# Optimization experiments

Measured on AMD Instinct MI355X. Metric: run time of the kernel, lower is better.

## Reference

```python
import jax, jax.numpy as jnp
import numpy as np

NEG_SLOPE = 0.2

def gat_conv(x, edge_index, W, a_src, a_dst, b, heads, out_ch, concat):
    # PyG GATConv (add_self_loops=True, eval mode / no dropout)
    N = x.shape[0]
    loop = jnp.arange(N, dtype=edge_index.dtype)
    src = jnp.concatenate([edge_index[0], loop])
    dst = jnp.concatenate([edge_index[1], loop])
    h = (x @ W.T).reshape(N, heads, out_ch)            # [N,H,C]
    alpha_s = (h * a_src).sum(-1)                      # [N,H]
    alpha_d = (h * a_dst).sum(-1)                      # [N,H]
    e = jax.nn.leaky_relu(alpha_s[src] + alpha_d[dst], NEG_SLOPE)  # [E,H]
    # segment softmax over incoming edges of each dst node
    m = jax.ops.segment_max(e, dst, num_segments=N)
    e = jnp.exp(e - m[dst])
    denom = jax.ops.segment_sum(e, dst, num_segments=N)
    alpha = e / (denom[dst] + 1e-16)                   # [E,H]
    msg = h[src] * alpha[..., None]                    # [E,H,C]
    out = jax.ops.segment_sum(msg, dst, num_segments=N)  # [N,H,C]
    out = out.reshape(N, heads * out_ch) if concat else out.mean(axis=1)
    return out + b


def setup_inputs() -> dict:
    key = jax.random.key(0)
    ks = jax.random.split(key, 16)
    N, E, F_in, HID, H, OUT = 20000, 320000, 512, 256, 8, 128
    C = HID // H  # 32 channels per head
    x = jax.random.normal(ks[0], (N, F_in), dtype=jnp.float32)
    edge_index = jax.random.randint(ks[1], (2, E), 0, N, dtype=jnp.int32)
    s = 0.05
    inp = {
        'x': x, 'edge_index': edge_index,
        # layer 0: F_in -> H*C, concat
        'W0': jax.random.normal(ks[2], (H * C, F_in)) * s,
        'a_src0': jax.random.normal(ks[3], (1, H, C)) * s,
        'a_dst0': jax.random.normal(ks[4], (1, H, C)) * s,
        'b0': jnp.zeros((H * C,), jnp.float32),
        # layer 1: H*C -> H*C, concat
        'W1': jax.random.normal(ks[5], (H * C, H * C)) * s,
        'a_src1': jax.random.normal(ks[6], (1, H, C)) * s,
        'a_dst1': jax.random.normal(ks[7], (1, H, C)) * s,
        'b1': jnp.zeros((H * C,), jnp.float32),
        # layer 2: H*C -> OUT, 1 head, concat=False
        'W2': jax.random.normal(ks[8], (OUT, H * C)) * s,
        'a_src2': jax.random.normal(ks[9], (1, 1, OUT)) * s,
        'a_dst2': jax.random.normal(ks[10], (1, 1, OUT)) * s,
        'b2': jnp.zeros((OUT,), jnp.float32),
    }
    return inp


def reference(x, edge_index, W0, a_src0, a_dst0, b0, W1, a_src1, a_dst1, b1,
              W2, a_src2, a_dst2, b2):
    H, C, OUT = 8, 32, 128
    h = gat_conv(x, edge_index, W0, a_src0, a_dst0, b0, H, C, True)
    h = jax.nn.relu(h)
    h = gat_conv(h, edge_index, W1, a_src1, a_dst1, b1, H, C, True)
    h = jax.nn.relu(h)
    h_pen = h  # h_list[-1]
    h = gat_conv(h, edge_index, W2, a_src2, a_dst2, b2, 1, OUT, False)
    return (h_pen, h)
```

## Files before the change

### kernel.cpp

```cpp
#include <hip/hip_runtime.h>
#include <hip/hip_bf16.h>


using bf16 = __hip_bfloat16;

typedef __attribute__((ext_vector_type(8))) short bf16x8;
typedef __attribute__((ext_vector_type(4))) short short4v;
typedef __attribute__((ext_vector_type(4))) float f32x4;
typedef __attribute__((ext_vector_type(2))) float f32x2;
typedef __attribute__((ext_vector_type(2))) unsigned int uint2v;

__device__ __forceinline__ float u2f(unsigned u) { union { float f; unsigned u; } c; c.u = u; return c.f; }
__device__ __forceinline__ unsigned f2u(float x) { union { float f; unsigned u; } c; c.f = x; return c.u; }
__device__ __forceinline__ short bfbits(float x) {
  unsigned xu = f2u(x);
  return (short)((xu + 0x7FFF + ((xu >> 16) & 1)) >> 16);
}

__global__ void hist_kernel(const int* __restrict__ ei, int E, int N, int* __restrict__ cnt) {
  int e = blockIdx.x * 256 + threadIdx.x;
  if (e >= E + N) return;
  int dst = (e < E) ? ei[E + e] : (e - E);
  atomicAdd(&cnt[dst], 1);
}

__global__ __launch_bounds__(1024) void scan_kernel(const int* __restrict__ cnt,
                                                    int* __restrict__ row_start, int N) {
  __shared__ int part[1024];
  int t = threadIdx.x;
  int chunk = (N + 1023) / 1024;
  int lo = t * chunk; if (lo > N) lo = N;
  int hi = lo + chunk; if (hi > N) hi = N;
  int s = 0;
  for (int i = lo; i < hi; ++i) s += cnt[i];
  part[t] = s;
  __syncthreads();
  for (int off = 1; off < 1024; off <<= 1) {
    int add = (t >= off) ? part[t - off] : 0;
    __syncthreads();
    part[t] += add;
    __syncthreads();
  }
  int run = part[t] - s;
  for (int i = lo; i < hi; ++i) { row_start[i] = run; run += cnt[i]; }
  if (t == 1023) row_start[N] = part[1023];
}

__global__ void scatter_kernel(const int* __restrict__ ei, int E, int N,
                               const int* __restrict__ row_start, int* __restrict__ cursor,
                               int* __restrict__ csr_src) {
  int e = blockIdx.x * 256 + threadIdx.x;
  if (e >= E + N) return;
  int src, dst;
  if (e < E) { src = ei[e]; dst = ei[E + e]; }
  else       { src = e - E; dst = e - E; }
  int pos = atomicAdd(&cursor[dst], 1);
  csr_src[row_start[dst] + pos] = src;
}

__global__ void split3_kernel(const float* __restrict__ W0, const float* __restrict__ W1,
                              const float* __restrict__ W2,
                              unsigned short* __restrict__ W0h, unsigned short* __restrict__ W0l,
                              unsigned short* __restrict__ W1h, unsigned short* __restrict__ W1l,
                              unsigned short* __restrict__ W2h, unsigned short* __restrict__ W2l,
                              int n0_4, int n1_4, int n2_4) {
  int i = blockIdx.x * 256 + threadIdx.x;
  const float* in; unsigned short *hi, *lo; int idx;
  if (i < n0_4)                { in = W0; hi = W0h; lo = W0l; idx = i; }
  else if (i < n0_4 + n1_4)    { in = W1; hi = W1h; lo = W1l; idx = i - n0_4; }
  else if (i < n0_4 + n1_4 + n2_4) { in = W2; hi = W2h; lo = W2l; idx = i - n0_4 - n1_4; }
  else return;
  f32x4 v = *(const f32x4*)(in + (size_t)idx * 4);
  short4v h, l;
#pragma unroll
  for (int k = 0; k < 4; ++k) {
    short hb = bfbits(v[k]);
    h[k] = hb;
    l[k] = bfbits(v[k] - u2f(((unsigned)(unsigned short)hb) << 16));
  }
  *(short4v*)(hi + (size_t)idx * 4) = h;
  *(short4v*)(lo + (size_t)idx * 4) = l;
}

#define LDP 40

__device__ __forceinline__ bf16x8 make_frag(const short* S, int row, int g) {
  short4v klo = *(const short4v*)&S[row * LDP + g * 4];
  short4v khi = *(const short4v*)&S[row * LDP + 16 + g * 4];
  bf16x8 r;
#pragma unroll
  for (int i = 0; i < 4; ++i) { r[i] = klo[i]; r[i + 4] = khi[i]; }
  return r;
}

template <bool FUSE8, bool WF32>
__global__ __launch_bounds__(256) void gemm_mfma(const float* __restrict__ Af,
                                                 const unsigned short* __restrict__ Bhg,
                                                 const unsigned short* __restrict__ Blg,
                                                 const float* __restrict__ Asrc,
                                                 const float* __restrict__ Adst,
                                                 float* __restrict__ as_,
                                                 float* __restrict__ ad_,
                                                 float* __restrict__ C,
                                                 unsigned short* __restrict__ C16,
                                                 int M, int Nn, int K, int NB) {
  int id = blockIdx.x;
  int r8 = id & 7;
  int q  = id >> 3;
  int bn = q % NB;
  int bm = r8 + 8 * (q / NB);
  if (bm * 64 >= M) return;

  __shared__ short Ah[64 * LDP];
  __shared__ short Al[64 * LDP];
  __shared__ short Bh[64 * LDP];
  __shared__ short Bl[64 * LDP];
  int t = threadIdx.x;
  int w = t >> 6, l = t & 63;
  int g = l >> 4, lr = l & 15;

  f32x4 acc[4];
#pragma unroll
  for (int j = 0; j < 4; ++j) acc[j] = (f32x4)(0.f);

  int srow = t >> 2;
  int sseg = (t & 3) * 8;
  int gm = bm * 64 + srow;
  int gn = bn * 64 + srow;
  const float* Abase = Af + (size_t)gm * K + sseg;
  const unsigned short* Bhb = Bhg + (size_t)gn * K + sseg;
  const unsigned short* Blb = Blg + (size_t)gn * K + sseg;

  f32x4 va0 = (f32x4)(0.f), va1 = (f32x4)(0.f);
  int4 vbh, vbl;
  vbh = *(const int4*)(Bhb);
  vbl = *(const int4*)(Blb);
  if (gm < M) { va0 = *(const f32x4*)(Abase); va1 = *(const f32x4*)(Abase + 4); }

  for (int kt = 0; kt < K; kt += 32) {
    short4v h0, l0, h1, l1;
#pragma unroll
    for (int i = 0; i < 4; ++i) {
      short hb0 = bfbits(va0[i]);
      l0[i] = bfbits(va0[i] - u2f(((unsigned)(unsigned short)hb0) << 16));
      h0[i] = hb0;
      short hb1 = bfbits(va1[i]);
      l1[i] = bfbits(va1[i] - u2f(((unsigned)(unsigned short)hb1) << 16));
      h1[i] = hb1;
    }
    __syncthreads();
    *(int4*)&Bh[srow * LDP + sseg] = vbh;
    *(int4*)&Bl[srow * LDP + sseg] = vbl;
    *(short4v*)&Ah[srow * LDP + sseg]     = h0;
    *(short4v*)&Ah[srow * LDP + sseg + 4] = h1;
    *(short4v*)&Al[srow * LDP + sseg]     = l0;
    *(short4v*)&Al[srow * LDP + sseg + 4] = l1;
    __syncthreads();

    if (kt + 32 < K) {
      int k2 = kt + 32;
      vbh = *(const int4*)(Bhb + k2);
      vbl = *(const int4*)(Blb + k2);
      if (gm < M) { va0 = *(const f32x4*)(Abase + k2); va1 = *(const f32x4*)(Abase + k2 + 4); }
    }

    int arow = w * 16 + lr;
    bf16x8 ah = make_frag(Ah, arow, g);
    bf16x8 al = make_frag(Al, arow, g);
#pragma unroll
    for (int j = 0; j < 4; ++j) {
      int brow = j * 16 + lr;
      bf16x8 bh = make_frag(Bh, brow, g);
      bf16x8 bl = make_frag(Bl, brow, g);
      acc[j] = __builtin_amdgcn_mfma_f32_16x16x32_bf16(ah, bh, acc[j], 0, 0, 0);
      acc[j] = __builtin_amdgcn_mfma_f32_16x16x32_bf16(al, bh, acc[j], 0, 0, 0);
      acc[j] = __builtin_amdgcn_mfma_f32_16x16x32_bf16(ah, bl, acc[j], 0, 0, 0);
    }
  }

#pragma unroll
  for (int j = 0; j < 4; ++j) {
#pragma unroll
    for (int r = 0; r < 4; ++r) {
      int row = bm * 64 + w * 16 + g * 4 + r;
      int col = bn * 64 + j * 16 + lr;
      if (row < M) {
        float v = acc[j][r];
        if constexpr (WF32) C[(size_t)row * Nn + col] = v;
        C16[(size_t)row * Nn + col] = (unsigned short)bfbits(v);
      }
    }
  }

  if constexpr (FUSE8) {
    float cs[4], cd[4];
#pragma unroll
    for (int j = 0; j < 4; ++j) {
      cs[j] = Asrc[bn * 64 + j * 16 + lr];
      cd[j] = Adst[bn * 64 + j * 16 + lr];
    }
#pragma unroll
    for (int r = 0; r < 4; ++r) {
      float sA0 = acc[0][r] * cs[0] + acc[1][r] * cs[1];
      float sA1 = acc[2][r] * cs[2] + acc[3][r] * cs[3];
      float sD0 = acc[0][r] * cd[0] + acc[1][r] * cd[1];
      float sD1 = acc[2][r] * cd[2] + acc[3][r] * cd[3];
#pragma unroll
      for (int mask = 1; mask < 16; mask <<= 1) {
        sA0 += __shfl_xor(sA0, mask);
        sA1 += __shfl_xor(sA1, mask);
        sD0 += __shfl_xor(sD0, mask);
        sD1 += __shfl_xor(sD1, mask);
      }
      if (lr == 0) {
        int row = bm * 64 + w * 16 + g * 4 + r;
        if (row < M) {
          as_[row * 8 + bn * 2]     = sA0;
          as_[row * 8 + bn * 2 + 1] = sA1;
          ad_[row * 8 + bn * 2]     = sD0;
          ad_[row * 8 + bn * 2 + 1] = sD1;
        }
      }
    }
  }
}

template <int H, int C>
__global__ __launch_bounds__(64) void alpha_kernel(const float* __restrict__ Hb,
                                                   const float* __restrict__ a_src,
                                                   const float* __restrict__ a_dst,
                                                   float* __restrict__ as_,
                                                   float* __restrict__ ad_, int N) {
  constexpr int HC = H * C;
  constexpr int EPL = HC / 64;
  constexpr int LPH = 64 / H;
  int n = blockIdx.x;
  int l = threadIdx.x;
  const float* row = Hb + (size_t)n * HC + l * EPL;
  float s1 = 0.f, s2 = 0.f;
  if constexpr (EPL == 4) {
    f32x4 v = *(const f32x4*)row;
    f32x4 a1 = *(const f32x4*)(a_src + l * 4);
    f32x4 a2 = *(const f32x4*)(a_dst + l * 4);
#pragma unroll
    for (int k = 0; k < 4; ++k) { s1 += v[k] * a1[k]; s2 += v[k] * a2[k]; }
  } else {
    f32x2 v = *(const f32x2*)row;
    f32x2 a1 = *(const f32x2*)(a_src + l * 2);
    f32x2 a2 = *(const f32x2*)(a_dst + l * 2);
#pragma unroll
    for (int k = 0; k < 2; ++k) { s1 += v[k] * a1[k]; s2 += v[k] * a2[k]; }
  }
#pragma unroll
  for (int mask = 1; mask < LPH; mask <<= 1) {
    s1 += __shfl_xor(s1, mask);
    s2 += __shfl_xor(s2, mask);
  }
  if ((l & (LPH - 1)) == 0) {
    int h = l / LPH;
    as_[n * H + h] = s1;
    ad_[n * H + h] = s2;
  }
}

template <int H, int C, bool RELU>
__global__ __launch_bounds__(64) void agg_kernel(const unsigned short* __restrict__ Hb16,
                                                 const float* __restrict__ as_,
                                                 const float* __restrict__ ad_,
                                                 const int* __restrict__ row_start,
                                                 const int* __restrict__ csr_src,
                                                 const float* __restrict__ bias,
                                                 float* __restrict__ out, int N) {
  int n = blockIdx.x;
  if (n >= N) return;
  int l = threadIdx.x;
  int s = row_start[n], e = row_start[n + 1];

  constexpr int LPH = 64 / H;
  constexpr int CPL = C / LPH;
  constexpr int HC = H * C;
  int h2 = l / LPH;
  int cb = (l % LPH) * CPL;
  float ad2 = ad_[n * H + h2];

  float acc[CPL];
#pragma unroll
  for (int c = 0; c < CPL; ++c) acc[c] = 0.f;
  float denom = 0.f;

  int j = s;
  for (; j + 1 < e; j += 2) {
    int s0 = csr_src[j], s1v = csr_src[j + 1];
    float x0 = as_[s0 * H + h2] + ad2;
    float x1 = as_[s1v * H + h2] + ad2;
    x0 = x0 > 0.f ? x0 : 0.2f * x0;
    x1 = x1 > 0.f ? x1 : 0.2f * x1;
    float p0 = __expf(x0), p1 = __expf(x1);
    denom += p0 + p1;
    const unsigned short* hp0 = Hb16 + (size_t)s0 * HC + h2 * C + cb;
    const unsigned short* hp1 = Hb16 + (size_t)s1v * HC + h2 * C + cb;
    if constexpr (CPL == 4) {
      uint2v u0 = *(const uint2v*)hp0;
      uint2v u1 = *(const uint2v*)hp1;
#pragma unroll
      for (int c = 0; c < 2; ++c) {
        acc[2 * c]     += p0 * u2f(u0[c] << 16)         + p1 * u2f(u1[c] << 16);
        acc[2 * c + 1] += p0 * u2f(u0[c] & 0xFFFF0000u) + p1 * u2f(u1[c] & 0xFFFF0000u);
      }
    } else {
      unsigned u0 = *(const unsigned*)hp0;
      unsigned u1 = *(const unsigned*)hp1;
      acc[0] += p0 * u2f(u0 << 16)         + p1 * u2f(u1 << 16);
      acc[1] += p0 * u2f(u0 & 0xFFFF0000u) + p1 * u2f(u1 & 0xFFFF0000u);
    }
  }
  if (j < e) {
    int s0 = csr_src[j];
    float x0 = as_[s0 * H + h2] + ad2;
    x0 = x0 > 0.f ? x0 : 0.2f * x0;
    float p0 = __expf(x0);
    denom += p0;
    const unsigned short* hp0 = Hb16 + (size_t)s0 * HC + h2 * C + cb;
    if constexpr (CPL == 4) {
      uint2v u0 = *(const uint2v*)hp0;
#pragma unroll
      for (int c = 0; c < 2; ++c) {
        acc[2 * c]     += p0 * u2f(u0[c] << 16);
        acc[2 * c + 1] += p0 * u2f(u0[c] & 0xFFFF0000u);
      }
    } else {
      unsigned u0 = *(const unsigned*)hp0;
      acc[0] += p0 * u2f(u0 << 16);
      acc[1] += p0 * u2f(u0 & 0xFFFF0000u);
    }
  }

  float inv = 1.f / (denom + 1e-16f);
#pragma unroll
  for (int c = 0; c < CPL; ++c) {
    float v = acc[c] * inv + bias[h2 * C + cb + c];
    if (RELU) v = fmaxf(v, 0.f);
    out[(size_t)n * HC + h2 * C + cb + c] = v;
  }
}

extern "C" void kernel_launch(void* const* d_in, const int* in_sizes, int n_in,
                              void* d_out, int out_size, void* d_ws, size_t ws_size,
                              hipStream_t stream) {
  const float* x    = (const float*)d_in[0];
  const int*   ei   = (const int*)d_in[1];
  const float* W0   = (const float*)d_in[2];
  const float* asr0 = (const float*)d_in[3];
  const float* adt0 = (const float*)d_in[4];
  const float* b0   = (const float*)d_in[5];
  const float* W1   = (const float*)d_in[6];
  const float* asr1 = (const float*)d_in[7];
  const float* adt1 = (const float*)d_in[8];
  const float* b1   = (const float*)d_in[9];
  const float* W2   = (const float*)d_in[10];
  const float* asr2 = (const float*)d_in[11];
  const float* adt2 = (const float*)d_in[12];
  const float* b2   = (const float*)d_in[13];

  const int FIN = 512, HID = 256, OUTC = 128;
  int N = in_sizes[0] / FIN;
  int E = in_sizes[1] / 2;
  int Etot = E + N;

  char* ws = (char*)d_ws;
  size_t off = 0;
  auto alloc = [&](size_t bytes) -> void* {
    void* p = ws + off;
    off = (off + bytes + 255) & ~(size_t)255;
    return p;
  };
  int* cnt       = (int*)alloc((size_t)N * 4);
  int* cursor    = (int*)alloc((size_t)N * 4);
  int* row_start = (int*)alloc((size_t)(N + 1) * 4);
  int* csr_src   = (int*)alloc((size_t)Etot * 4);
  float* as_     = (float*)alloc((size_t)N * 8 * 4);
  float* ad_     = (float*)alloc((size_t)N * 8 * 4);
  float* Hb      = (float*)alloc((size_t)N * HID * 4);
  unsigned short* Hb16 = (unsigned short*)alloc((size_t)N * HID * 2);
  float* act     = (float*)alloc((size_t)N * HID * 4);
  unsigned short* W0h = (unsigned short*)alloc((size_t)HID * FIN * 2);
  unsigned short* W0l = (unsigned short*)alloc((size_t)HID * FIN * 2);
  unsigned short* W1h = (unsigned short*)alloc((size_t)HID * HID * 2);
  unsigned short* W1l = (unsigned short*)alloc((size_t)HID * HID * 2);
  unsigned short* W2h = (unsigned short*)alloc((size_t)OUTC * HID * 2);
  unsigned short* W2l = (unsigned short*)alloc((size_t)OUTC * HID * 2);

  float* hpen = (float*)d_out;
  float* out2 = (float*)d_out + (size_t)N * HID;

  int n0_4 = HID * FIN / 4, n1_4 = HID * HID / 4, n2_4 = OUTC * HID / 4;
  int nsplit = n0_4 + n1_4 + n2_4;
  split3_kernel<<<(nsplit + 255) / 256, 256, 0, stream>>>(W0, W1, W2, W0h, W0l, W1h, W1l,
                                                          W2h, W2l, n0_4, n1_4, n2_4);

  (void)hipMemsetAsync(cnt, 0, (size_t)((char*)cursor - (char*)cnt) + (size_t)N * 4, stream);
  int eb = (Etot + 255) / 256;
  hist_kernel<<<eb, 256, 0, stream>>>(ei, E, N, cnt);
  scan_kernel<<<1, 1024, 0, stream>>>(cnt, row_start, N);
  scatter_kernel<<<eb, 256, 0, stream>>>(ei, E, N, row_start, cursor, csr_src);

  int mb = (N + 63) / 64;
  int mb8 = (mb + 7) / 8;
  int grid4 = 8 * 4 * mb8;
  int grid2 = 8 * 2 * mb8;

  gemm_mfma<true, false><<<grid4, 256, 0, stream>>>(x, W0h, W0l, asr0, adt0, as_, ad_,
                                                    nullptr, Hb16, N, HID, FIN, 4);
  agg_kernel<8, 32, true><<<N, 64, 0, stream>>>(Hb16, as_, ad_, row_start, csr_src, b0,
                                                act, N);

  gemm_mfma<true, false><<<grid4, 256, 0, stream>>>(act, W1h, W1l, asr1, adt1, as_, ad_,
                                                    nullptr, Hb16, N, HID, HID, 4);
  agg_kernel<8, 32, true><<<N, 64, 0, stream>>>(Hb16, as_, ad_, row_start, csr_src, b1,
                                                hpen, N);

  gemm_mfma<false, true><<<grid2, 256, 0, stream>>>(hpen, W2h, W2l, nullptr, nullptr,
                                                    nullptr, nullptr, Hb, Hb16,
                                                    N, OUTC, HID, 2);
  alpha_kernel<1, 128><<<N, 64, 0, stream>>>(Hb, asr2, adt2, as_, ad_, N);
  agg_kernel<1, 128, false><<<N, 64, 0, stream>>>(Hb16, as_, ad_, row_start, csr_src, b2,
                                                  out2, N);
}
```

Measured before the change: 230.6 us.

## Fuse layer-2 attention logits into GEMM epilogue via atomics; unroll aggregation by four

The last-layer GEMM now computes per-row source and destination attention dot products in its epilogue and accumulates them with atomicAdd across the two column blocks. This removes the fp32 output write, the separate alpha kernel and its reread of that buffer. Small zeroing kernels are added before the GEMM to clear the accumulators. The aggregation loop is also unrolled from 2 to 4 edges per step to expose more memory-level parallelism, at the cost of more registers. Accumulating with atomics makes the summation order nondeterministic.

```diff
diff --git a/kernel.cpp b/kernel.cpp
--- a/kernel.cpp
+++ b/kernel.cpp
@@ -82,6 +82,11 @@
   *(short4v*)(lo + (size_t)idx * 4) = l;
 }
 
+__global__ void zero_f32_kernel(float* __restrict__ p, int n) {
+  int i = blockIdx.x * 256 + threadIdx.x;
+  if (i < n) p[i] = 0.f;
+}
+
 #define LDP 40
 
 __device__ __forceinline__ bf16x8 make_frag(const short* S, int row, int g) {
@@ -93,7 +98,7 @@
   return r;
 }
 
-template <bool FUSE8, bool WF32>
+template <bool FUSE8, bool FUSE1>
 __global__ __launch_bounds__(256) void gemm_mfma(const float* __restrict__ Af,
                                                  const unsigned short* __restrict__ Bhg,
                                                  const unsigned short* __restrict__ Blg,
@@ -101,7 +106,6 @@
                                                  const float* __restrict__ Adst,
                                                  float* __restrict__ as_,
                                                  float* __restrict__ ad_,
-                                                 float* __restrict__ C,
                                                  unsigned short* __restrict__ C16,
                                                  int M, int Nn, int K, int NB) {
   int id = blockIdx.x;
@@ -132,9 +136,8 @@
   const unsigned short* Blb = Blg + (size_t)gn * K + sseg;
 
   f32x4 va0 = (f32x4)(0.f), va1 = (f32x4)(0.f);
-  int4 vbh, vbl;
-  vbh = *(const int4*)(Bhb);
-  vbl = *(const int4*)(Blb);
+  int4 vbh = *(const int4*)(Bhb);
+  int4 vbl = *(const int4*)(Blb);
   if (gm < M) { va0 = *(const f32x4*)(Abase); va1 = *(const f32x4*)(Abase + 4); }
 
   for (int kt = 0; kt < K; kt += 32) {
@@ -184,11 +187,7 @@
     for (int r = 0; r < 4; ++r) {
       int row = bm * 64 + w * 16 + g * 4 + r;
       int col = bn * 64 + j * 16 + lr;
-      if (row < M) {
-        float v = acc[j][r];
-        if constexpr (WF32) C[(size_t)row * Nn + col] = v;
-        C16[(size_t)row * Nn + col] = (unsigned short)bfbits(v);
-      }
+      if (row < M) C16[(size_t)row * Nn + col] = (unsigned short)bfbits(acc[j][r]);
     }
   }
 
@@ -223,43 +222,31 @@
       }
     }
   }
-}
-
-template <int H, int C>
-__global__ __launch_bounds__(64) void alpha_kernel(const float* __restrict__ Hb,
-                                                   const float* __restrict__ a_src,
-                                                   const float* __restrict__ a_dst,
-                                                   float* __restrict__ as_,
-                                                   float* __restrict__ ad_, int N) {
-  constexpr int HC = H * C;
-  constexpr int EPL = HC / 64;
-  constexpr int LPH = 64 / H;
-  int n = blockIdx.x;
-  int l = threadIdx.x;
-  const float* row = Hb + (size_t)n * HC + l * EPL;
-  float s1 = 0.f, s2 = 0.f;
-  if constexpr (EPL == 4) {
-    f32x4 v = *(const f32x4*)row;
-    f32x4 a1 = *(const f32x4*)(a_src + l * 4);
-    f32x4 a2 = *(const f32x4*)(a_dst + l * 4);
-#pragma unroll
-    for (int k = 0; k < 4; ++k) { s1 += v[k] * a1[k]; s2 += v[k] * a2[k]; }
-  } else {
-    f32x2 v = *(const f32x2*)row;
-    f32x2 a1 = *(const f32x2*)(a_src + l * 2);
-    f32x2 a2 = *(const f32x2*)(a_dst + l * 2);
-#pragma unroll
-    for (int k = 0; k < 2; ++k) { s1 += v[k] * a1[k]; s2 += v[k] * a2[k]; }
-  }
-#pragma unroll
-  for (int mask = 1; mask < LPH; mask <<= 1) {
-    s1 += __shfl_xor(s1, mask);
-    s2 += __shfl_xor(s2, mask);
-  }
-  if ((l & (LPH - 1)) == 0) {
-    int h = l / LPH;
-    as_[n * H + h] = s1;
-    ad_[n * H + h] = s2;
+
+  if constexpr (FUSE1) {
+    float cs[4], cd[4];
+#pragma unroll
+    for (int j = 0; j < 4; ++j) {
+      cs[j] = Asrc[bn * 64 + j * 16 + lr];
+      cd[j] = Adst[bn * 64 + j * 16 + lr];
+    }
+#pragma unroll
+    for (int r = 0; r < 4; ++r) {
+      float sA = acc[0][r] * cs[0] + acc[1][r] * cs[1] + acc[2][r] * cs[2] + acc[3][r] * cs[3];
+      float sD = acc[0][r] * cd[0] + acc[1][r] * cd[1] + acc[2][r] * cd[2] + acc[3][r] * cd[3];
+#pragma unroll
+      for (int mask = 1; mask < 16; mask <<= 1) {
+        sA += __shfl_xor(sA, mask);
+        sD += __shfl_xor(sD, mask);
+      }
+      if (lr == 0) {
+        int row = bm * 64 + w * 16 + g * 4 + r;
+        if (row < M) {
+          atomicAdd(&as_[row], sA);
+          atomicAdd(&ad_[row], sD);
+        }
+      }
+    }
   }
 }
 
@@ -288,37 +275,46 @@
   for (int c = 0; c < CPL; ++c) acc[c] = 0.f;
   float denom = 0.f;
 
+  auto lrelu = [](float x) { return x > 0.f ? x : 0.2f * x; };
+
   int j = s;
-  for (; j + 1 < e; j += 2) {
-    int s0 = csr_src[j], s1v = csr_src[j + 1];
-    float x0 = as_[s0 * H + h2] + ad2;
-    float x1 = as_[s1v * H + h2] + ad2;
-    x0 = x0 > 0.f ? x0 : 0.2f * x0;
-    x1 = x1 > 0.f ? x1 : 0.2f * x1;
-    float p0 = __expf(x0), p1 = __expf(x1);
-    denom += p0 + p1;
+  for (; j + 3 < e; j += 4) {
+    int s0 = csr_src[j], s1 = csr_src[j + 1], s2 = csr_src[j + 2], s3 = csr_src[j + 3];
+    float x0 = as_[s0 * H + h2], x1 = as_[s1 * H + h2];
+    float x2 = as_[s2 * H + h2], x3 = as_[s3 * H + h2];
     const unsigned short* hp0 = Hb16 + (size_t)s0 * HC + h2 * C + cb;
-    const unsigned short* hp1 = Hb16 + (size_t)s1v * HC + h2 * C + cb;
+    const unsigned short* hp1 = Hb16 + (size_t)s1 * HC + h2 * C + cb;
+    const unsigned short* hp2 = Hb16 + (size_t)s2 * HC + h2 * C + cb;
+    const unsigned short* hp3 = Hb16 + (size_t)s3 * HC + h2 * C + cb;
+    float p0 = __expf(lrelu(x0 + ad2)), p1 = __expf(lrelu(x1 + ad2));
+    float p2 = __expf(lrelu(x2 + ad2)), p3 = __expf(lrelu(x3 + ad2));
+    denom += (p0 + p1) + (p2 + p3);
     if constexpr (CPL == 4) {
       uint2v u0 = *(const uint2v*)hp0;
       uint2v u1 = *(const uint2v*)hp1;
+      uint2v u2 = *(const uint2v*)hp2;
+      uint2v u3 = *(const uint2v*)hp3;
 #pragma unroll
       for (int c = 0; c < 2; ++c) {
-        acc[2 * c]     += p0 * u2f(u0[c] << 16)         + p1 * u2f(u1[c] << 16);
-        acc[2 * c + 1] += p0 * u2f(u0[c] & 0xFFFF0000u) + p1 * u2f(u1[c] & 0xFFFF0000u);
+        acc[2 * c]     += p0 * u2f(u0[c] << 16)         + p1 * u2f(u1[c] << 16)
+                        + p2 * u2f(u2[c] << 16)         + p3 * u2f(u3[c] << 16);
+        acc[2 * c + 1] += p0 * u2f(u0[c] & 0xFFFF0000u) + p1 * u2f(u1[c] & 0xFFFF0000u)
+                        + p2 * u2f(u2[c] & 0xFFFF0000u) + p3 * u2f(u3[c] & 0xFFFF0000u);
       }
     } else {
       unsigned u0 = *(const unsigned*)hp0;
       unsigned u1 = *(const unsigned*)hp1;
-      acc[0] += p0 * u2f(u0 << 16)         + p1 * u2f(u1 << 16);
-      acc[1] += p0 * u2f(u0 & 0xFFFF0000u) + p1 * u2f(u1 & 0xFFFF0000u);
-    }
-  }
-  if (j < e) {
+      unsigned u2 = *(const unsigned*)hp2;
+      unsigned u3 = *(const unsigned*)hp3;
+      acc[0] += p0 * u2f(u0 << 16)         + p1 * u2f(u1 << 16)
+              + p2 * u2f(u2 << 16)         + p3 * u2f(u3 << 16);
+      acc[1] += p0 * u2f(u0 & 0xFFFF0000u) + p1 * u2f(u1 & 0xFFFF0000u)
+              + p2 * u2f(u2 & 0xFFFF0000u) + p3 * u2f(u3 & 0xFFFF0000u);
+    }
+  }
+  for (; j < e; ++j) {
     int s0 = csr_src[j];
-    float x0 = as_[s0 * H + h2] + ad2;
-    x0 = x0 > 0.f ? x0 : 0.2f * x0;
-    float p0 = __expf(x0);
+    float p0 = __expf(lrelu(as_[s0 * H + h2] + ad2));
     denom += p0;
     const unsigned short* hp0 = Hb16 + (size_t)s0 * HC + h2 * C + cb;
     if constexpr (CPL == 4) {
@@ -380,7 +376,6 @@
   int* csr_src   = (int*)alloc((size_t)Etot * 4);
   float* as_     = (float*)alloc((size_t)N * 8 * 4);
   float* ad_     = (float*)alloc((size_t)N * 8 * 4);
-  float* Hb      = (float*)alloc((size_t)N * HID * 4);
   unsigned short* Hb16 = (unsigned short*)alloc((size_t)N * HID * 2);
   float* act     = (float*)alloc((size_t)N * HID * 4);
   unsigned short* W0h = (unsigned short*)alloc((size_t)HID * FIN * 2);
@@ -410,19 +405,19 @@
   int grid2 = 8 * 2 * mb8;
 
   gemm_mfma<true, false><<<grid4, 256, 0, stream>>>(x, W0h, W0l, asr0, adt0, as_, ad_,
-                                                    nullptr, Hb16, N, HID, FIN, 4);
+                                                    Hb16, N, HID, FIN, 4);
   agg_kernel<8, 32, true><<<N, 64, 0, stream>>>(Hb16, as_, ad_, row_start, csr_src, b0,
                                                 act, N);
 
   gemm_mfma<true, false><<<grid4, 256, 0, stream>>>(act, W1h, W1l, asr1, adt1, as_, ad_,
-                                                    nullptr, Hb16, N, HID, HID, 4);
+                                                    Hb16, N, HID, HID, 4);
   agg_kernel<8, 32, true><<<N, 64, 0, stream>>>(Hb16, as_, ad_, row_start, csr_src, b1,
                                                 hpen, N);
 
-  gemm_mfma<false, true><<<grid2, 256, 0, stream>>>(hpen, W2h, W2l, nullptr, nullptr,
-                                                    nullptr, nullptr, Hb, Hb16,
-                                                    N, OUTC, HID, 2);
-  alpha_kernel<1, 128><<<N, 64, 0, stream>>>(Hb, asr2, adt2, as_, ad_, N);
+  zero_f32_kernel<<<(2 * N + 255) / 256, 256, 0, stream>>>(as_, 2 * N);
+  zero_f32_kernel<<<(N + 255) / 256, 256, 0, stream>>>(ad_, N);
+  gemm_mfma<false, true><<<grid2, 256, 0, stream>>>(hpen, W2h, W2l, asr2, adt2, as_, ad_,
+                                                    Hb16, N, OUTC, HID, 2);
   agg_kernel<1, 128, false><<<N, 64, 0, stream>>>(Hb16, as_, ad_, row_start, csr_src, b2,
                                                   out2, N);
 }
```

New measurement: 223.5 us. -3.1%, faster.
